# Optimization experiments

Hardware: AMD Instinct MI355X
Metric: run time of the kernel (lower is better)

Reference implementation:

```python
import jax, jax.numpy as jnp
import numpy as np
from jax.scipy.linalg import expm

B = 524288      # batch of states (original module is per-vector; vmapped via batched matmuls)
IN = 64         # input_size
KDIM = 128      # koopman_size
W_PHI = (IN + KDIM) // 2   # 96, encoder MLP hidden width
W_INV = (KDIM + IN) // 2   # 96, decoder MLP hidden width


def setup_inputs() -> dict:
    key = jax.random.key(0)
    ks = jax.random.split(key, 8)
    def w(k, shape, fan_in):
        return jax.random.normal(k, shape, jnp.float32) / np.float32(np.sqrt(fan_in))
    return {
        "t": jnp.asarray(6.0, jnp.float32),                       # hours; module uses t/24
        "x": jax.random.normal(ks[0], (B, IN), jnp.float32),
        "A": jax.random.normal(ks[1], (KDIM, KDIM), jnp.float32) / np.float32(np.sqrt(KDIM)),
        "phi_W1": w(ks[2], (W_PHI, IN), IN),
        "phi_b1": jnp.zeros((W_PHI,), jnp.float32),
        "phi_W2": w(ks[3], (KDIM, W_PHI), W_PHI),                 # no final bias (skip=True)
        "inv_W1": w(ks[4], (W_INV, KDIM), KDIM),
        "inv_b1": jnp.zeros((W_INV,), jnp.float32),
        "inv_W2": w(ks[5], (IN, W_INV), W_INV),
        "inv_b2": jnp.zeros((IN,), jnp.float32),                  # use_final_bias=True (skip=False)
    }


def reference(t, x, A, phi_W1, phi_b1, phi_W2, inv_W1, inv_b1, inv_W2, inv_b2):
    # phi: z = C @ x + MLP(x), C = eye(KDIM, IN) -> zero-pad x into koopman space
    h = jax.nn.relu(x @ phi_W1.T + phi_b1)                # [B, W_PHI]
    z = jnp.pad(x, ((0, 0), (0, KDIM - IN))) + h @ phi_W2.T   # [B, KDIM]
    # Koopman propagation: K = expm(A * t/24); z <- K @ z (batched as z @ K.T)
    Kmat = expm(A * (t / 24.0), max_squarings=20)          # [KDIM, KDIM]
    z = z @ Kmat.T
    # phi_inv: plain MLP with final bias, no skip
    h2 = jax.nn.relu(z @ inv_W1.T + inv_b1)                # [B, W_INV]
    return h2 @ inv_W2.T + inv_b2                          # [B, IN]
```

## Files before the change

kernel.cpp:

```cpp
#include <hip/hip_runtime.h>

#define BTOT    524288
#define NT64    8192
#define GRID    512
#define TN      6

#define SX 72
#define SH 104
#define SZ 136

typedef __attribute__((ext_vector_type(8))) short s8v;
typedef __attribute__((ext_vector_type(4))) short s4v;
typedef __attribute__((ext_vector_type(4))) float f4v;

#define MFMA(a,b,c) __builtin_amdgcn_mfma_f32_16x16x32_bf16((a),(b),(c),0,0,0)
#define KEEP(x) asm volatile("" : "+v"(x))

__device__ __forceinline__ short f2b(float f) {
  union { float f; unsigned u; } v; v.f = f;
  unsigned r = v.u + 0x7fffu + ((v.u >> 16) & 1u);
  return (short)(r >> 16);
}
__device__ __forceinline__ float b2f(short s) {
  union { float f; unsigned u; } v; v.u = ((unsigned)(unsigned short)s) << 16;
  return v.f;
}
__device__ __forceinline__ s8v pack8(f4v u, f4v v) {
  s8v w;
  w[0] = f2b(u[0]); w[1] = f2b(u[1]); w[2] = f2b(u[2]); w[3] = f2b(u[3]);
  w[4] = f2b(v[0]); w[5] = f2b(v[1]); w[6] = f2b(v[2]); w[7] = f2b(v[3]);
  return w;
}
__device__ __forceinline__ s4v pack4(f4v a) {
  s4v w; w[0]=f2b(a[0]); w[1]=f2b(a[1]); w[2]=f2b(a[2]); w[3]=f2b(a[3]); return w;
}
__device__ __forceinline__ s4v pack4r(f4v a) {
  s4v w;
  w[0]=f2b(fmaxf(a[0],0.f)); w[1]=f2b(fmaxf(a[1],0.f));
  w[2]=f2b(fmaxf(a[2],0.f)); w[3]=f2b(fmaxf(a[3],0.f));
  return w;
}

__device__ __forceinline__ s8v ldfrag(const short* base, int row0, int kbase, int stride) {
  const int l = threadIdx.x & 63;
  return *(const s8v*)(base + (row0 + (l & 15)) * stride + kbase + (l >> 4) * 8);
}

__device__ __forceinline__ s8v ldact(const short* base, int col0, int kbase, int stride) {
  const int l = threadIdx.x & 63;
  return *(const s8v*)(base + (col0 + (l & 15)) * stride + kbase + (l >> 4) * 8);
}

#define WS_M1   0
#define WS_I1   8192
#define WS_W1   20480
#define WS_W2K  26624
#define WS_I2   38912

__device__ __forceinline__ int fragidx(int n, int k, int KS) {
  int jj = n >> 4, ks = k >> 5;
  int l = (n & 15) | (((k >> 3) & 3) << 4);
  return ((jj * KS + ks) * 64 + l) * 8 + (k & 7);
}

__global__ __launch_bounds__(512, 2) void koop_prep(
    const float* __restrict__ tptr, const float* __restrict__ Ag,
    const float* __restrict__ W2g, const float* __restrict__ w1g,
    const float* __restrict__ i1g, const float* __restrict__ i2g,
    short* __restrict__ wsp) {
  extern __shared__ __align__(16) char smem[];
  short* RThi = (short*)smem;
  short* RTlo = RThi + 128 * 136;
  float* sW2  = (float*)(RTlo + 128 * 136);
  float* sred = sW2 + 128 * 96;
  float* scratch = (float*)smem;

  const int tid = threadIdx.x;
  const int lane = tid & 63, wid = tid >> 6;
  const int c_ = lane & 15, g_ = lane >> 4;
  const int mr = wid * 16;

  for (int e = tid; e < 6144; e += 512)
    wsp[WS_W1 + fragidx(e >> 6, e & 63, 2)] = f2b(w1g[e]);
  for (int e = tid; e < 12288; e += 512)
    wsp[WS_I1 + fragidx(e >> 7, e & 127, 4)] = f2b(i1g[e]);
  for (int e = tid; e < 6144; e += 512)
    wsp[WS_I2 + fragidx(e / 96, e % 96, 3)] = f2b(i2g[e]);

  const float s = tptr[0] * (1.0f / 24.0f);
  for (int i = tid; i < 128 * 128; i += 512) scratch[i] = Ag[i] * s;
  for (int i = tid; i < 128 * 96;  i += 512) sW2[i] = W2g[i];
  __syncthreads();

  if (tid < 128) {
    float su = 0.f;
    for (int j = 0; j < 128; ++j) su += fabsf(scratch[tid * 128 + j]);
    sred[tid] = su;
  }
  __syncthreads();
  if (tid == 0) {
    float m = 0.f;
    for (int i = 0; i < 128; ++i) m = fmaxf(m, sred[i]);
    int j = 0; float sc = 1.f;
    while (m > 0.5f && j < 20) { m *= 0.5f; sc *= 0.5f; ++j; }
    sred[128] = (float)j; sred[129] = sc;
  }
  __syncthreads();
  const int jsq = (int)sred[128];
  const float sc = sred[129];

  s8v Ahi[4], Alo[4];
#pragma unroll
  for (int ks = 0; ks < 4; ++ks) {
    const float* p = scratch + (mr + c_) * 128 + ks * 32 + g_ * 8;
    f4v u = *(const f4v*)p, v = *(const f4v*)(p + 4);
    float vals[8] = {u[0], u[1], u[2], u[3], v[0], v[1], v[2], v[3]};
#pragma unroll
    for (int i = 0; i < 8; ++i) {
      float y = vals[i] * sc;
      short h = f2b(y);
      Ahi[ks][i] = h;
      Alo[ks][i] = f2b(y - b2f(h));
    }
  }
  float yv[32];
#pragma unroll
  for (int e = 0; e < 32; ++e) yv[e] = scratch[tid * 32 + e];
  __syncthreads();

#pragma unroll
  for (int e = 0; e < 32; ++e) {
    int idx = tid * 32 + e;
    int r = idx >> 7, c = idx & 127;
    float v = yv[e] * sc * (1.0f / TN) + ((r == c) ? 1.0f : 0.0f);
    short h = f2b(v);
    RThi[c * 136 + r] = h;
    RTlo[c * 136 + r] = f2b(v - b2f(h));
  }
  __syncthreads();

  for (int k = TN - 1; k >= 1; --k) {
    f4v acc[8];
#pragma unroll
    for (int nt = 0; nt < 8; ++nt) acc[nt] = (f4v){0.f, 0.f, 0.f, 0.f};
#pragma unroll
    for (int ks = 0; ks < 4; ++ks) {
#pragma unroll
      for (int nt = 0; nt < 8; ++nt) {
        s8v bh = ldfrag(RThi, nt * 16, ks * 32, 136);
        s8v bl = ldfrag(RTlo, nt * 16, ks * 32, 136);
        acc[nt] = MFMA(Ahi[ks], bh, acc[nt]);
        acc[nt] = MFMA(Alo[ks], bh, acc[nt]);
        acc[nt] = MFMA(Ahi[ks], bl, acc[nt]);
      }
    }
    __syncthreads();
    const float invk = 1.0f / (float)k;
#pragma unroll
    for (int nt = 0; nt < 8; ++nt)
#pragma unroll
      for (int r = 0; r < 4; ++r) {
        int row = mr + g_ * 4 + r, col = nt * 16 + c_;
        float v = acc[nt][r] * invk + ((row == col) ? 1.0f : 0.0f);
        short h = f2b(v);
        RThi[col * 136 + row] = h;
        RTlo[col * 136 + row] = f2b(v - b2f(h));
      }
    __syncthreads();
  }

  for (int it = 0; it < jsq; ++it) {
    s8v Shi[4], Slo[4];
#pragma unroll
    for (int ks = 0; ks < 4; ++ks) {
      int m = mr + c_;
      int k0 = ks * 32 + g_ * 8;
#pragma unroll
      for (int i = 0; i < 8; ++i) {
        Shi[ks][i] = RThi[(k0 + i) * 136 + m];
        Slo[ks][i] = RTlo[(k0 + i) * 136 + m];
      }
    }
    f4v acc[8];
#pragma unroll
    for (int nt = 0; nt < 8; ++nt) acc[nt] = (f4v){0.f, 0.f, 0.f, 0.f};
#pragma unroll
    for (int ks = 0; ks < 4; ++ks) {
#pragma unroll
      for (int nt = 0; nt < 8; ++nt) {
        s8v bh = ldfrag(RThi, nt * 16, ks * 32, 136);
        s8v bl = ldfrag(RTlo, nt * 16, ks * 32, 136);
        acc[nt] = MFMA(Shi[ks], bh, acc[nt]);
        acc[nt] = MFMA(Slo[ks], bh, acc[nt]);
        acc[nt] = MFMA(Shi[ks], bl, acc[nt]);
      }
    }
    __syncthreads();
#pragma unroll
    for (int nt = 0; nt < 8; ++nt)
#pragma unroll
      for (int r = 0; r < 4; ++r) {
        int row = mr + g_ * 4 + r, col = nt * 16 + c_;
        float v = acc[nt][r];
        short h = f2b(v);
        RThi[col * 136 + row] = h;
        RTlo[col * 136 + row] = f2b(v - b2f(h));
      }
    __syncthreads();
  }

  for (int e = tid; e < 128 * 64; e += 512) {
    int n = e >> 6, kk = e & 63;
    float v = b2f(RThi[kk * 136 + n]) + b2f(RTlo[kk * 136 + n]);
    wsp[WS_M1 + fragidx(n, kk, 2)] = f2b(v);
  }

  {
    s8v Shi[4], Slo[4];
#pragma unroll
    for (int ks = 0; ks < 4; ++ks) {
      int m = mr + c_;
      int k0 = ks * 32 + g_ * 8;
#pragma unroll
      for (int i = 0; i < 8; ++i) {
        Shi[ks][i] = RThi[(k0 + i) * 136 + m];
        Slo[ks][i] = RTlo[(k0 + i) * 136 + m];
      }
    }
    f4v acc[6];
#pragma unroll
    for (int nt = 0; nt < 6; ++nt) acc[nt] = (f4v){0.f, 0.f, 0.f, 0.f};
#pragma unroll
    for (int ks = 0; ks < 4; ++ks) {
#pragma unroll
      for (int nt = 0; nt < 6; ++nt) {
        s8v bh, bl;
#pragma unroll
        for (int i = 0; i < 8; ++i) {
          float v = sW2[(ks * 32 + g_ * 8 + i) * 96 + nt * 16 + c_];
          short h = f2b(v);
          bh[i] = h;
          bl[i] = f2b(v - b2f(h));
        }
        acc[nt] = MFMA(Shi[ks], bh, acc[nt]);
        acc[nt] = MFMA(Slo[ks], bh, acc[nt]);
        acc[nt] = MFMA(Shi[ks], bl, acc[nt]);
      }
    }
#pragma unroll
    for (int nt = 0; nt < 6; ++nt)
#pragma unroll
      for (int r = 0; r < 4; ++r)
        wsp[WS_W2K + fragidx(mr + g_ * 4 + r, nt * 16 + c_, 3)] = f2b(acc[nt][r]);
  }
}

__global__ __launch_bounds__(256, 2) void koop_main(
    const float* __restrict__ xg, const float* __restrict__ b1g,
    const float* __restrict__ bi1g, const float* __restrict__ bi2g,
    const short* __restrict__ wsp, float* __restrict__ outg) {
  extern __shared__ __align__(16) char smem[];
  short* sM1f = (short*)smem;
  short* sI1f = sM1f + 8192;
  short* sX   = sI1f + 12288;
  short* sH   = sX + 64 * SX;
  short* sZ   = sH + 64 * SH;

  const int tid = threadIdx.x;
  const int lane = tid & 63, wid = tid >> 6;
  const int c_ = lane & 15, g_ = lane >> 4;
  const int bg = wid >> 1, fg = wid & 1;

  for (int i = tid; i < 20480 / 8; i += 256)
    ((f4v*)sM1f)[i] = ((const f4v*)(wsp + WS_M1))[i];

  f4v wW1[3][2], wW2K[4][3], wI2[2][3];
  f4v bW1[3], bI1[3], bI2[2];
#pragma unroll
  for (int fb = 0; fb < 3; ++fb) {
    bW1[fb] = *(const f4v*)(b1g  + (fg * 3 + fb) * 16 + g_ * 4);  KEEP(bW1[fb]);
    bI1[fb] = *(const f4v*)(bi1g + (fg * 3 + fb) * 16 + g_ * 4);  KEEP(bI1[fb]);
#pragma unroll
    for (int ks = 0; ks < 2; ++ks) {
      wW1[fb][ks] = *(const f4v*)(wsp + WS_W1 + (((fg * 3 + fb) * 2 + ks) * 64 + lane) * 8);
      KEEP(wW1[fb][ks]);
    }
  }
#pragma unroll
  for (int fb = 0; fb < 4; ++fb)
#pragma unroll
    for (int ks = 0; ks < 3; ++ks) {
      wW2K[fb][ks] = *(const f4v*)(wsp + WS_W2K + (((fg * 4 + fb) * 3 + ks) * 64 + lane) * 8);
      KEEP(wW2K[fb][ks]);
    }
#pragma unroll
  for (int fb = 0; fb < 2; ++fb) {
    bI2[fb] = *(const f4v*)(bi2g + (fg * 2 + fb) * 16 + g_ * 4);  KEEP(bI2[fb]);
#pragma unroll
    for (int ks = 0; ks < 3; ++ks) {
      wI2[fb][ks] = *(const f4v*)(wsp + WS_I2 + (((fg * 2 + fb) * 3 + ks) * 64 + lane) * 8);
      KEEP(wI2[fb][ks]);
    }
  }

  const int xr = tid >> 2, xq = tid & 3;

  int tile = blockIdx.x;
  {
    const float* src = xg + ((size_t)tile * 64 + xr) * 64 + xq * 16;
    *(s8v*)(sX + xr * SX + xq * 16) = pack8(*(const f4v*)src, *(const f4v*)(src + 4));
    *(s8v*)(sX + xr * SX + xq * 16 + 8) = pack8(*(const f4v*)(src + 8), *(const f4v*)(src + 12));
  }
  __syncthreads();

  for (; tile < NT64; tile += GRID) {
    const int nxt = tile + GRID;
    f4v pv0, pv1, pv2, pv3;
    if (nxt < NT64) {
      const float* src = xg + ((size_t)nxt * 64 + xr) * 64 + xq * 16;
      pv0 = *(const f4v*)src;       pv1 = *(const f4v*)(src + 4);
      pv2 = *(const f4v*)(src + 8); pv3 = *(const f4v*)(src + 12);
    }

    s8v bx[2][2];
#pragma unroll
    for (int bb = 0; bb < 2; ++bb) {
      const int col0 = (bg * 2 + bb) * 16;
      bx[bb][0] = ldact(sX, col0, 0, SX);
      bx[bb][1] = ldact(sX, col0, 32, SX);
#pragma unroll
      for (int fb = 0; fb < 3; ++fb) {
        f4v acc = bW1[fb];
        acc = MFMA(__builtin_bit_cast(s8v, wW1[fb][0]), bx[bb][0], acc);
        acc = MFMA(__builtin_bit_cast(s8v, wW1[fb][1]), bx[bb][1], acc);
        *(s4v*)(sH + (col0 + c_) * SH + (fg * 3 + fb) * 16 + g_ * 4) = pack4r(acc);
      }
    }
    __syncthreads();

    if (nxt < NT64) {
      *(s8v*)(sX + xr * SX + xq * 16) = pack8(pv0, pv1);
      *(s8v*)(sX + xr * SX + xq * 16 + 8) = pack8(pv2, pv3);
    }

    s8v m1f[4][2];
#pragma unroll
    for (int fb = 0; fb < 4; ++fb)
#pragma unroll
      for (int ks = 0; ks < 2; ++ks)
        m1f[fb][ks] = *(const s8v*)(sM1f + (((fg * 4 + fb) * 2 + ks) * 64 + lane) * 8);
#pragma unroll
    for (int bb = 0; bb < 2; ++bb) {
      const int col0 = (bg * 2 + bb) * 16;
      s8v hb0 = ldact(sH, col0, 0, SH);
      s8v hb1 = ldact(sH, col0, 32, SH);
      s8v hb2 = ldact(sH, col0, 64, SH);
#pragma unroll
      for (int fb = 0; fb < 4; ++fb) {
        f4v acc = (f4v){0.f, 0.f, 0.f, 0.f};
        acc = MFMA(m1f[fb][0], bx[bb][0], acc);
        acc = MFMA(m1f[fb][1], bx[bb][1], acc);
        acc = MFMA(__builtin_bit_cast(s8v, wW2K[fb][0]), hb0, acc);
        acc = MFMA(__builtin_bit_cast(s8v, wW2K[fb][1]), hb1, acc);
        acc = MFMA(__builtin_bit_cast(s8v, wW2K[fb][2]), hb2, acc);
        *(s4v*)(sZ + (col0 + c_) * SZ + (fg * 4 + fb) * 16 + g_ * 4) = pack4(acc);
      }
    }
    __syncthreads();

    s8v i1f[3][4];
#pragma unroll
    for (int fb = 0; fb < 3; ++fb)
#pragma unroll
      for (int ks = 0; ks < 4; ++ks)
        i1f[fb][ks] = *(const s8v*)(sI1f + (((fg * 3 + fb) * 4 + ks) * 64 + lane) * 8);
#pragma unroll
    for (int bb = 0; bb < 2; ++bb) {
      const int col0 = (bg * 2 + bb) * 16;
      s8v zb[4];
#pragma unroll
      for (int ks = 0; ks < 4; ++ks) zb[ks] = ldact(sZ, col0, ks * 32, SZ);
#pragma unroll
      for (int fb = 0; fb < 3; ++fb) {
        f4v acc = bI1[fb];
#pragma unroll
        for (int ks = 0; ks < 4; ++ks) acc = MFMA(i1f[fb][ks], zb[ks], acc);
        *(s4v*)(sH + (col0 + c_) * SH + (fg * 3 + fb) * 16 + g_ * 4) = pack4r(acc);
      }
    }
    __syncthreads();

#pragma unroll
    for (int bb = 0; bb < 2; ++bb) {
      const int col0 = (bg * 2 + bb) * 16;
      s8v h0 = ldact(sH, col0, 0, SH);
      s8v h1 = ldact(sH, col0, 32, SH);
      s8v h2 = ldact(sH, col0, 64, SH);
#pragma unroll
      for (int fb = 0; fb < 2; ++fb) {
        f4v acc = bI2[fb];
        acc = MFMA(__builtin_bit_cast(s8v, wI2[fb][0]), h0, acc);
        acc = MFMA(__builtin_bit_cast(s8v, wI2[fb][1]), h1, acc);
        acc = MFMA(__builtin_bit_cast(s8v, wI2[fb][2]), h2, acc);
        *(f4v*)(outg + ((size_t)tile * 64 + col0 + c_) * 64 + (fg * 2 + fb) * 16 + g_ * 4) = acc;
      }
    }
    __syncthreads();
  }
}

#define PREP_LDS (128 * 136 * 2 * 2 + 128 * 96 * 4 + 130 * 4)
#define MAIN_LDS ((8192 + 12288 + 64 * SX + 64 * SH + 64 * SZ) * 2)

extern "C" void kernel_launch(void* const* d_in, const int* in_sizes, int n_in,
                              void* d_out, int out_size, void* d_ws, size_t ws_size,
                              hipStream_t stream) {
  (void)in_sizes; (void)n_in; (void)out_size; (void)ws_size;
  const float* t     = (const float*)d_in[0];
  const float* x     = (const float*)d_in[1];
  const float* A     = (const float*)d_in[2];
  const float* phiW1 = (const float*)d_in[3];
  const float* phib1 = (const float*)d_in[4];
  const float* phiW2 = (const float*)d_in[5];
  const float* invW1 = (const float*)d_in[6];
  const float* invb1 = (const float*)d_in[7];
  const float* invW2 = (const float*)d_in[8];
  const float* invb2 = (const float*)d_in[9];
  float* out = (float*)d_out;
  short* wsp = (short*)d_ws;

  (void)hipFuncSetAttribute((const void*)koop_prep,
                            hipFuncAttributeMaxDynamicSharedMemorySize, PREP_LDS);
  (void)hipFuncSetAttribute((const void*)koop_main,
                            hipFuncAttributeMaxDynamicSharedMemorySize, MAIN_LDS);

  koop_prep<<<1, 512, PREP_LDS, stream>>>(t, A, phiW2, phiW1, invW1, invW2, wsp);
  koop_main<<<GRID, 256, MAIN_LDS, stream>>>(x, phib1, invb1, invb2, wsp, out);
}
```

Before: 139.6 us.

## Give each wave its own 32-row tile and drop block-wide barriers in main kernel

The main kernel is restructured so each wave independently processes 32-row tiles through all four layers, with per-wave swizzled LDS activation buffers. This removes the four __syncthreads per tile and the cross-wave split of feature blocks. Each wave now holds all W1, W2K and I2 fragments in registers at 512 threads and one block per CU, which raises register pressure. The direct x load no longer has the previous prefetch overlap. The prep kernel's norm reduction is also parallelised with shuffles and a log2-based squaring count.

```diff
diff --git a/kernel.cpp b/kernel.cpp
--- a/kernel.cpp
+++ b/kernel.cpp
@@ -1,13 +1,7 @@
 #include <hip/hip_runtime.h>
 
 #define BTOT    524288
-#define NT64    8192
-#define GRID    512
 #define TN      6
-
-#define SX 72
-#define SH 104
-#define SZ 136
 
 typedef __attribute__((ext_vector_type(8))) short s8v;
 typedef __attribute__((ext_vector_type(4))) short s4v;
@@ -15,6 +9,7 @@
 
 #define MFMA(a,b,c) __builtin_amdgcn_mfma_f32_16x16x32_bf16((a),(b),(c),0,0,0)
 #define KEEP(x) asm volatile("" : "+v"(x))
+#define BC(x) __builtin_bit_cast(s8v, x)
 
 __device__ __forceinline__ short f2b(float f) {
   union { float f; unsigned u; } v; v.f = f;
@@ -45,10 +40,8 @@
   const int l = threadIdx.x & 63;
   return *(const s8v*)(base + (row0 + (l & 15)) * stride + kbase + (l >> 4) * 8);
 }
-
-__device__ __forceinline__ s8v ldact(const short* base, int col0, int kbase, int stride) {
-  const int l = threadIdx.x & 63;
-  return *(const s8v*)(base + (col0 + (l & 15)) * stride + kbase + (l >> 4) * 8);
+__device__ __forceinline__ s8v ldw(const short* base, int chunk) {
+  return *(const s8v*)(base + (chunk * 64 + (threadIdx.x & 63)) * 8);
 }
 
 #define WS_M1   0
@@ -92,18 +85,29 @@
   for (int i = tid; i < 128 * 96;  i += 512) sW2[i] = W2g[i];
   __syncthreads();
 
-  if (tid < 128) {
+  {
+    const int row = tid >> 2, q = tid & 3;
     float su = 0.f;
-    for (int j = 0; j < 128; ++j) su += fabsf(scratch[tid * 128 + j]);
-    sred[tid] = su;
-  }
-  __syncthreads();
-  if (tid == 0) {
-    float m = 0.f;
-    for (int i = 0; i < 128; ++i) m = fmaxf(m, sred[i]);
-    int j = 0; float sc = 1.f;
-    while (m > 0.5f && j < 20) { m *= 0.5f; sc *= 0.5f; ++j; }
-    sred[128] = (float)j; sred[129] = sc;
+    const float* rp = scratch + row * 128 + q * 32;
+#pragma unroll 8
+    for (int j = 0; j < 32; ++j) su += fabsf(rp[j]);
+    su += __shfl_xor(su, 1);
+    su += __shfl_xor(su, 2);
+    if (q == 0) sred[row] = su;
+  }
+  __syncthreads();
+  if (tid < 64) {
+    float m = fmaxf(sred[tid], sred[tid + 64]);
+#pragma unroll
+    for (int d = 32; d; d >>= 1) m = fmaxf(m, __shfl_xor(m, d));
+    if (tid == 0) {
+      int j = 0;
+      if (m > 0.5f) {
+        j = (int)ceilf(log2f(m * 2.0f));
+        if (j < 0) j = 0; if (j > 20) j = 20;
+      }
+      sred[128] = (float)j; sred[129] = exp2f(-(float)j);
+    }
   }
   __syncthreads();
   const int jsq = (int)sred[128];
@@ -255,162 +259,151 @@
   }
 }
 
-__global__ __launch_bounds__(256, 2) void koop_main(
+__global__ __launch_bounds__(512, 1) void koop_main(
     const float* __restrict__ xg, const float* __restrict__ b1g,
     const float* __restrict__ bi1g, const float* __restrict__ bi2g,
     const short* __restrict__ wsp, float* __restrict__ outg) {
   extern __shared__ __align__(16) char smem[];
-  short* sM1f = (short*)smem;
-  short* sI1f = sM1f + 8192;
-  short* sX   = sI1f + 12288;
-  short* sH   = sX + 64 * SX;
-  short* sZ   = sH + 64 * SH;
-
-  const int tid = threadIdx.x;
-  const int lane = tid & 63, wid = tid >> 6;
+  short* sWf = (short*)smem;
+  float* sB  = (float*)(smem + 40960);
+  char*  actB = smem + 41984 + (threadIdx.x >> 6) * 14336;
+
+  const int tid = threadIdx.x, lane = tid & 63, wid = tid >> 6;
   const int c_ = lane & 15, g_ = lane >> 4;
-  const int bg = wid >> 1, fg = wid & 1;
-
-  for (int i = tid; i < 20480 / 8; i += 256)
-    ((f4v*)sM1f)[i] = ((const f4v*)(wsp + WS_M1))[i];
-
-  f4v wW1[3][2], wW2K[4][3], wI2[2][3];
-  f4v bW1[3], bI1[3], bI2[2];
-#pragma unroll
-  for (int fb = 0; fb < 3; ++fb) {
-    bW1[fb] = *(const f4v*)(b1g  + (fg * 3 + fb) * 16 + g_ * 4);  KEEP(bW1[fb]);
-    bI1[fb] = *(const f4v*)(bi1g + (fg * 3 + fb) * 16 + g_ * 4);  KEEP(bI1[fb]);
+
+  for (int i = tid; i < 2560; i += 512)
+    ((f4v*)sWf)[i] = ((const f4v*)(wsp + WS_M1))[i];
+  if (tid < 96) sB[tid] = b1g[tid];
+  else if (tid < 192) sB[tid] = bi1g[tid - 96];
+  else if (tid < 256) sB[tid] = bi2g[tid - 192];
+
+  f4v W1v[6][2], W2Kv[8][3], I2v[4][3];
+#pragma unroll
+  for (int fb = 0; fb < 6; ++fb)
 #pragma unroll
     for (int ks = 0; ks < 2; ++ks) {
-      wW1[fb][ks] = *(const f4v*)(wsp + WS_W1 + (((fg * 3 + fb) * 2 + ks) * 64 + lane) * 8);
-      KEEP(wW1[fb][ks]);
-    }
-  }
+      W1v[fb][ks] = *(const f4v*)(wsp + WS_W1 + ((fb * 2 + ks) * 64 + lane) * 8);
+      KEEP(W1v[fb][ks]);
+    }
+#pragma unroll
+  for (int fb = 0; fb < 8; ++fb)
+#pragma unroll
+    for (int ks = 0; ks < 3; ++ks) {
+      W2Kv[fb][ks] = *(const f4v*)(wsp + WS_W2K + ((fb * 3 + ks) * 64 + lane) * 8);
+      KEEP(W2Kv[fb][ks]);
+    }
 #pragma unroll
   for (int fb = 0; fb < 4; ++fb)
 #pragma unroll
     for (int ks = 0; ks < 3; ++ks) {
-      wW2K[fb][ks] = *(const f4v*)(wsp + WS_W2K + (((fg * 4 + fb) * 3 + ks) * 64 + lane) * 8);
-      KEEP(wW2K[fb][ks]);
-    }
-#pragma unroll
-  for (int fb = 0; fb < 2; ++fb) {
-    bI2[fb] = *(const f4v*)(bi2g + (fg * 2 + fb) * 16 + g_ * 4);  KEEP(bI2[fb]);
-#pragma unroll
-    for (int ks = 0; ks < 3; ++ks) {
-      wI2[fb][ks] = *(const f4v*)(wsp + WS_I2 + (((fg * 2 + fb) * 3 + ks) * 64 + lane) * 8);
-      KEEP(wI2[fb][ks]);
-    }
-  }
-
-  const int xr = tid >> 2, xq = tid & 3;
-
-  int tile = blockIdx.x;
-  {
-    const float* src = xg + ((size_t)tile * 64 + xr) * 64 + xq * 16;
-    *(s8v*)(sX + xr * SX + xq * 16) = pack8(*(const f4v*)src, *(const f4v*)(src + 4));
-    *(s8v*)(sX + xr * SX + xq * 16 + 8) = pack8(*(const f4v*)(src + 8), *(const f4v*)(src + 12));
-  }
-  __syncthreads();
-
-  for (; tile < NT64; tile += GRID) {
-    const int nxt = tile + GRID;
-    f4v pv0, pv1, pv2, pv3;
-    if (nxt < NT64) {
-      const float* src = xg + ((size_t)nxt * 64 + xr) * 64 + xq * 16;
-      pv0 = *(const f4v*)src;       pv1 = *(const f4v*)(src + 4);
-      pv2 = *(const f4v*)(src + 8); pv3 = *(const f4v*)(src + 12);
-    }
+      I2v[fb][ks] = *(const f4v*)(wsp + WS_I2 + ((fb * 3 + ks) * 64 + lane) * 8);
+      KEEP(I2v[fb][ks]);
+    }
+  __syncthreads();
+
+  const int wgid = blockIdx.x * 8 + wid;
+  for (int it = 0; it < 8; ++it) {
+    const size_t r0 = ((size_t)(it * 2048 + wgid)) * 32;
 
     s8v bx[2][2];
 #pragma unroll
+    for (int bb = 0; bb < 2; ++bb)
+#pragma unroll
+      for (int ks = 0; ks < 2; ++ks) {
+        const float* p = xg + (r0 + bb * 16 + c_) * 64 + ks * 32 + g_ * 8;
+        bx[bb][ks] = pack8(*(const f4v*)p, *(const f4v*)(p + 4));
+      }
+
+#pragma unroll
+    for (int fb = 0; fb < 6; ++fb) {
+      f4v bias = *(const f4v*)(sB + fb * 16 + g_ * 4);
+#pragma unroll
+      for (int bb = 0; bb < 2; ++bb) {
+        f4v acc = bias;
+        acc = MFMA(BC(W1v[fb][0]), bx[bb][0], acc);
+        acc = MFMA(BC(W1v[fb][1]), bx[bb][1], acc);
+        const int r = bb * 16 + c_;
+        *(s4v*)(actB + ((r * 192 + fb * 32 + g_ * 8) ^ ((r & 3) << 4))) = pack4r(acc);
+      }
+    }
+
+    s8v hb[2][3];
+#pragma unroll
     for (int bb = 0; bb < 2; ++bb) {
-      const int col0 = (bg * 2 + bb) * 16;
-      bx[bb][0] = ldact(sX, col0, 0, SX);
-      bx[bb][1] = ldact(sX, col0, 32, SX);
-#pragma unroll
-      for (int fb = 0; fb < 3; ++fb) {
-        f4v acc = bW1[fb];
-        acc = MFMA(__builtin_bit_cast(s8v, wW1[fb][0]), bx[bb][0], acc);
-        acc = MFMA(__builtin_bit_cast(s8v, wW1[fb][1]), bx[bb][1], acc);
-        *(s4v*)(sH + (col0 + c_) * SH + (fg * 3 + fb) * 16 + g_ * 4) = pack4r(acc);
-      }
-    }
-    __syncthreads();
-
-    if (nxt < NT64) {
-      *(s8v*)(sX + xr * SX + xq * 16) = pack8(pv0, pv1);
-      *(s8v*)(sX + xr * SX + xq * 16 + 8) = pack8(pv2, pv3);
-    }
-
-    s8v m1f[4][2];
-#pragma unroll
-    for (int fb = 0; fb < 4; ++fb)
-#pragma unroll
-      for (int ks = 0; ks < 2; ++ks)
-        m1f[fb][ks] = *(const s8v*)(sM1f + (((fg * 4 + fb) * 2 + ks) * 64 + lane) * 8);
+      const int r = bb * 16 + c_;
+#pragma unroll
+      for (int ks = 0; ks < 3; ++ks)
+        hb[bb][ks] = *(const s8v*)(actB + ((r * 192 + ks * 64 + g_ * 16) ^ ((r & 3) << 4)));
+    }
+#pragma unroll
+    for (int fb = 0; fb < 8; ++fb) {
+      s8v m0 = ldw(sWf, fb * 2 + 0);
+      s8v m1 = ldw(sWf, fb * 2 + 1);
+#pragma unroll
+      for (int bb = 0; bb < 2; ++bb) {
+        f4v acc = (f4v){0.f, 0.f, 0.f, 0.f};
+        acc = MFMA(m0, bx[bb][0], acc);
+        acc = MFMA(m1, bx[bb][1], acc);
+        acc = MFMA(BC(W2Kv[fb][0]), hb[bb][0], acc);
+        acc = MFMA(BC(W2Kv[fb][1]), hb[bb][1], acc);
+        acc = MFMA(BC(W2Kv[fb][2]), hb[bb][2], acc);
+        const int r = bb * 16 + c_;
+        *(s4v*)(actB + 6144 + ((r * 256 + fb * 32 + g_ * 8) ^ ((r & 7) << 4))) = pack4(acc);
+      }
+    }
+
+    s8v zb[2][4];
 #pragma unroll
     for (int bb = 0; bb < 2; ++bb) {
-      const int col0 = (bg * 2 + bb) * 16;
-      s8v hb0 = ldact(sH, col0, 0, SH);
-      s8v hb1 = ldact(sH, col0, 32, SH);
-      s8v hb2 = ldact(sH, col0, 64, SH);
-#pragma unroll
-      for (int fb = 0; fb < 4; ++fb) {
-        f4v acc = (f4v){0.f, 0.f, 0.f, 0.f};
-        acc = MFMA(m1f[fb][0], bx[bb][0], acc);
-        acc = MFMA(m1f[fb][1], bx[bb][1], acc);
-        acc = MFMA(__builtin_bit_cast(s8v, wW2K[fb][0]), hb0, acc);
-        acc = MFMA(__builtin_bit_cast(s8v, wW2K[fb][1]), hb1, acc);
-        acc = MFMA(__builtin_bit_cast(s8v, wW2K[fb][2]), hb2, acc);
-        *(s4v*)(sZ + (col0 + c_) * SZ + (fg * 4 + fb) * 16 + g_ * 4) = pack4(acc);
-      }
-    }
-    __syncthreads();
-
-    s8v i1f[3][4];
-#pragma unroll
-    for (int fb = 0; fb < 3; ++fb)
+      const int r = bb * 16 + c_;
 #pragma unroll
       for (int ks = 0; ks < 4; ++ks)
-        i1f[fb][ks] = *(const s8v*)(sI1f + (((fg * 3 + fb) * 4 + ks) * 64 + lane) * 8);
+        zb[bb][ks] = *(const s8v*)(actB + 6144 + ((r * 256 + ks * 64 + g_ * 16) ^ ((r & 7) << 4)));
+    }
+#pragma unroll
+    for (int fb = 0; fb < 6; ++fb) {
+      s8v i0 = ldw(sWf + 8192, fb * 4 + 0);
+      s8v i1 = ldw(sWf + 8192, fb * 4 + 1);
+      s8v i2 = ldw(sWf + 8192, fb * 4 + 2);
+      s8v i3 = ldw(sWf + 8192, fb * 4 + 3);
+      f4v bias = *(const f4v*)(sB + 96 + fb * 16 + g_ * 4);
+#pragma unroll
+      for (int bb = 0; bb < 2; ++bb) {
+        f4v acc = bias;
+        acc = MFMA(i0, zb[bb][0], acc);
+        acc = MFMA(i1, zb[bb][1], acc);
+        acc = MFMA(i2, zb[bb][2], acc);
+        acc = MFMA(i3, zb[bb][3], acc);
+        const int r = bb * 16 + c_;
+        *(s4v*)(actB + 6144 + ((r * 256 + fb * 32 + g_ * 8) ^ ((r & 7) << 4))) = pack4r(acc);
+      }
+    }
+
+    s8v h2[2][3];
 #pragma unroll
     for (int bb = 0; bb < 2; ++bb) {
-      const int col0 = (bg * 2 + bb) * 16;
-      s8v zb[4];
-#pragma unroll
-      for (int ks = 0; ks < 4; ++ks) zb[ks] = ldact(sZ, col0, ks * 32, SZ);
-#pragma unroll
-      for (int fb = 0; fb < 3; ++fb) {
-        f4v acc = bI1[fb];
-#pragma unroll
-        for (int ks = 0; ks < 4; ++ks) acc = MFMA(i1f[fb][ks], zb[ks], acc);
-        *(s4v*)(sH + (col0 + c_) * SH + (fg * 3 + fb) * 16 + g_ * 4) = pack4r(acc);
-      }
-    }
-    __syncthreads();
-
-#pragma unroll
-    for (int bb = 0; bb < 2; ++bb) {
-      const int col0 = (bg * 2 + bb) * 16;
-      s8v h0 = ldact(sH, col0, 0, SH);
-      s8v h1 = ldact(sH, col0, 32, SH);
-      s8v h2 = ldact(sH, col0, 64, SH);
-#pragma unroll
-      for (int fb = 0; fb < 2; ++fb) {
-        f4v acc = bI2[fb];
-        acc = MFMA(__builtin_bit_cast(s8v, wI2[fb][0]), h0, acc);
-        acc = MFMA(__builtin_bit_cast(s8v, wI2[fb][1]), h1, acc);
-        acc = MFMA(__builtin_bit_cast(s8v, wI2[fb][2]), h2, acc);
-        *(f4v*)(outg + ((size_t)tile * 64 + col0 + c_) * 64 + (fg * 2 + fb) * 16 + g_ * 4) = acc;
-      }
-    }
-    __syncthreads();
+      const int r = bb * 16 + c_;
+#pragma unroll
+      for (int ks = 0; ks < 3; ++ks)
+        h2[bb][ks] = *(const s8v*)(actB + 6144 + ((r * 256 + ks * 64 + g_ * 16) ^ ((r & 7) << 4)));
+    }
+#pragma unroll
+    for (int fb = 0; fb < 4; ++fb) {
+      f4v bias = *(const f4v*)(sB + 192 + fb * 16 + g_ * 4);
+#pragma unroll
+      for (int bb = 0; bb < 2; ++bb) {
+        f4v acc = bias;
+        acc = MFMA(BC(I2v[fb][0]), h2[bb][0], acc);
+        acc = MFMA(BC(I2v[fb][1]), h2[bb][1], acc);
+        acc = MFMA(BC(I2v[fb][2]), h2[bb][2], acc);
+        *(f4v*)(outg + (r0 + bb * 16 + c_) * 64 + fb * 16 + g_ * 4) = acc;
+      }
+    }
   }
 }
 
 #define PREP_LDS (128 * 136 * 2 * 2 + 128 * 96 * 4 + 130 * 4)
-#define MAIN_LDS ((8192 + 12288 + 64 * SX + 64 * SH + 64 * SZ) * 2)
+#define MAIN_LDS (41984 + 8 * 14336)
 
 extern "C" void kernel_launch(void* const* d_in, const int* in_sizes, int n_in,
                               void* d_out, int out_size, void* d_ws, size_t ws_size,
@@ -435,5 +428,5 @@
                             hipFuncAttributeMaxDynamicSharedMemorySize, MAIN_LDS);
 
   koop_prep<<<1, 512, PREP_LDS, stream>>>(t, A, phiW2, phiW1, invW1, invW2, wsp);
-  koop_main<<<GRID, 256, MAIN_LDS, stream>>>(x, phib1, invb1, invb2, wsp, out);
-}
+  koop_main<<<256, 512, MAIN_LDS, stream>>>(x, phib1, invb1, invb2, wsp, out);
+}
```

After: 204.9 us. +46.7%, slower.
